# Optimization experiments

Hardware: AMD Instinct MI355X
Metric: run time of the kernel (lower is better)

The kernel has to match this reference:

```python
import jax, jax.numpy as jnp
import numpy as np

N = 100000
E = 1600000
H = 128
C = 40
BN_EPS = 1e-5


def setup_inputs() -> dict:
    key = jax.random.key(0)
    ks = jax.random.split(key, 8)
    x = jax.random.normal(ks[0], (N, H), dtype=jnp.float32)
    edge_index = jax.random.randint(ks[1], (2, E), 0, N, dtype=jnp.int64)
    # 3 GCN blocks (input + 2 hidden), all [H -> H] since in_channels == hidden_channels
    bn_gamma = jnp.ones((3, H), dtype=jnp.float32)
    bn_beta = jnp.zeros((3, H), dtype=jnp.float32)
    W = jax.random.normal(ks[2], (3, H, H), dtype=jnp.float32) / np.sqrt(H)
    b = jnp.zeros((3, H), dtype=jnp.float32)
    Wo = jax.random.normal(ks[3], (H, C), dtype=jnp.float32) / np.sqrt(H)
    bo = jnp.zeros((C,), dtype=jnp.float32)
    return {"x": x, "edge_index": edge_index, "bn_gamma": bn_gamma,
            "bn_beta": bn_beta, "W": W, "b": b, "Wo": Wo, "bo": bo}


def _gcn_norm(edge_index):
    # add self-loops, compute symmetric normalization deg^-1/2 * deg^-1/2
    loop = jnp.arange(N, dtype=edge_index.dtype)
    src = jnp.concatenate([edge_index[0], loop])  # [E+N]
    dst = jnp.concatenate([edge_index[1], loop])
    deg = jax.ops.segment_sum(jnp.ones_like(dst, dtype=jnp.float32), dst, num_segments=N)
    dinv = jnp.where(deg > 0, jax.lax.rsqrt(deg), 0.0)
    norm = dinv[src] * dinv[dst]  # [E+N]
    return src, dst, norm


def _block(x, src, dst, norm, gamma, beta, Wl, bl):
    # Dropout(p=0.6) in eval mode -> identity
    # BatchNorm (batch statistics, biased var, eps=1e-5)
    mean = jnp.mean(x, axis=0)
    var = jnp.mean(jnp.square(x - mean), axis=0)
    x = gamma * (x - mean) * jax.lax.rsqrt(var + BN_EPS) + beta
    # GCNConv: linear transform then normalized scatter-add aggregation
    h = x @ Wl  # [N, H]
    msg = h[src] * norm[:, None]  # [E+N, H] gather + scale
    out = jax.ops.segment_sum(msg, dst, num_segments=N) + bl
    return jax.nn.relu(out)


def reference(x, edge_index, bn_gamma, bn_beta, W, b, Wo, bo):
    src, dst, norm = _gcn_norm(edge_index)
    for i in range(3):
        x = _block(x, src, dst, norm, bn_gamma[i], bn_beta[i], W[i], b[i])
    logits = x @ Wo + bo  # [N, C]
    return jnp.squeeze(logits)
```

## Files before the change

kernel.cpp:

```cpp
#include <hip/hip_runtime.h>
#include <hip/hip_bf16.h>
#include <hip/hip_fp16.h>
#include <cstdint>

#define HDIM 128
#define BN_EPS 1e-5f
#define SCAN_CHUNK 1024

typedef _Float16 hf2 __attribute__((ext_vector_type(2)));
typedef _Float16 hf8 __attribute__((ext_vector_type(8)));
typedef float f32x4 __attribute__((ext_vector_type(4)));

static inline size_t align256(size_t x) { return (x + 255) & ~size_t(255); }

__global__ void detect_kernel(const int* __restrict__ ebuf, int* __restrict__ flag) {
    __shared__ int r[256];
    int tid = threadIdx.x;
    int o = 0;
    for (int i = tid; i < 4096; i += 256) o |= ebuf[2 * i + 1];
    r[tid] = o;
    __syncthreads();
    for (int s = 128; s > 0; s >>= 1) {
        if (tid < s) r[tid] |= r[tid + s];
        __syncthreads();
    }
    if (tid == 0) *flag = (r[0] == 0) ? 1 : 0;
}

__device__ __forceinline__ void bn_finalize_body(int blk, int t,
                                                 const float* __restrict__ part, int rows,
                                                 const float* __restrict__ gamma,
                                                 const float* __restrict__ beta,
                                                 const float* __restrict__ W,
                                                 _Float16* __restrict__ Wf,
                                                 float* __restrict__ hbp, int n) {
    int c = t & 127, h = t >> 7;
    float s = 0.f, s2 = 0.f;
    for (int b = h; b < rows; b += 2) {
        float2 v = ((const float2*)part)[(size_t)b * 128 + c];
        s += v.x; s2 += v.y;
    }
    __shared__ float rS[2][HDIM], rQ[2][HDIM];
    __shared__ float scs[HDIM], shs[HDIM];
    rS[h][c] = s; rQ[h][c] = s2;
    __syncthreads();
    if (h == 0) {
        s += rS[1][c]; s2 += rQ[1][c];
        float mean = s / n;
        float var = s2 / n - mean * mean;
        float sc = gamma[c] * rsqrtf(var + BN_EPS);
        scs[c] = sc;
        shs[c] = beta[c] - mean * sc;
    }
    __syncthreads();
    float acc = 0.f;
    int tbase = (c >> 4) * 4;
    int nlane = c & 15;
    int k0 = blk * 16 + h * 8;
#pragma unroll
    for (int kk = 0; kk < 8; ++kk) {
        int k = k0 + kk;
        float w = W[k * HDIM + c];
        int idx = (((tbase + (k >> 5)) * 64) + (((k >> 3) & 3) * 16 + nlane)) * 8 + (k & 7);
        Wf[idx] = (_Float16)(scs[k] * w);
        acc += shs[k] * w;
    }
    hbp[(blk * 2 + h) * HDIM + c] = acc;
}

__global__ __launch_bounds__(256) void front_kernel(const int* __restrict__ ebuf,
                                                    const int* __restrict__ flag,
                                                    int* __restrict__ deg,
                                                    int* __restrict__ rank,
                                                    const float4* __restrict__ x4,
                                                    float* __restrict__ part,
                                                    int E, int n, int ge, int nbn) {
    int t = threadIdx.x;
    if ((int)blockIdx.x < ge) {
        int e = blockIdx.x * 256 + t;
        if (e >= E) return;
        int d = (*flag) ? ebuf[2 * (E + e)] : ebuf[E + e];
        rank[e] = atomicAdd(&deg[d], 1);
        return;
    }
    int b = blockIdx.x - ge;
    int c4 = t & 31;
    int rsub = t >> 5;
    int rowsPer = (n + nbn - 1) / nbn;
    int r0 = b * rowsPer, r1 = min(r0 + rowsPer, n);
    float s[4] = {0.f, 0.f, 0.f, 0.f}, q[4] = {0.f, 0.f, 0.f, 0.f};
    for (int r = r0 + rsub; r < r1; r += 8) {
        float4 v = x4[(size_t)r * 32 + c4];
        s[0] += v.x; q[0] += v.x * v.x;
        s[1] += v.y; q[1] += v.y * v.y;
        s[2] += v.z; q[2] += v.z * v.z;
        s[3] += v.w; q[3] += v.w * v.w;
    }
    __shared__ float sS[8][HDIM], sQ[8][HDIM];
#pragma unroll
    for (int j = 0; j < 4; ++j) { sS[rsub][c4 * 4 + j] = s[j]; sQ[rsub][c4 * 4 + j] = q[j]; }
    __syncthreads();
    if (t < HDIM) {
        float ss = 0.f, qq = 0.f;
#pragma unroll
        for (int k = 0; k < 8; ++k) { ss += sS[k][t]; qq += sQ[k][t]; }
        ((float2*)part)[(size_t)b * 128 + t] = make_float2(ss, qq);
    }
}

__global__ __launch_bounds__(256) void bn_reduce1(const float* __restrict__ part,
                                                  float* __restrict__ part2, int rows) {
    int t = threadIdx.x;
    int per = (rows + gridDim.x - 1) / gridDim.x;
    int b0 = blockIdx.x * per, b1 = min(b0 + per, rows);
    float acc = 0.f;
    for (int r = b0; r < b1; ++r) acc += part[(size_t)r * 256 + t];
    part2[(size_t)blockIdx.x * 256 + t] = acc;
}

__global__ __launch_bounds__(256) void scanp_fin(const int* __restrict__ deg,
                                                 int* __restrict__ bsum,
                                                 const float* __restrict__ part2, int rows,
                                                 const float* __restrict__ gamma,
                                                 const float* __restrict__ beta,
                                                 const float* __restrict__ W,
                                                 _Float16* __restrict__ Wf,
                                                 float* __restrict__ hbp,
                                                 int n, int nscan) {
    int t = threadIdx.x;
    if ((int)blockIdx.x < nscan) {
        int base = blockIdx.x * SCAN_CHUNK;
        int lane = t & 63, w = t >> 6;
        int s = 0;
#pragma unroll
        for (int i = 0; i < 4; ++i) {
            int idx = base + t + 256 * i;
            if (idx < n) s += deg[idx];
        }
#pragma unroll
        for (int off = 32; off > 0; off >>= 1) s += __shfl_down(s, off);
        __shared__ int wred[4];
        if (lane == 0) wred[w] = s;
        __syncthreads();
        if (t == 0) bsum[blockIdx.x] = wred[0] + wred[1] + wred[2] + wred[3];
        return;
    }
    bn_finalize_body(blockIdx.x - nscan, t, part2, rows, gamma, beta, W, Wf, hbp, n);
}

__global__ __launch_bounds__(256) void bn_finalize_k(const float* __restrict__ part, int rows,
                                                     const float* __restrict__ gamma,
                                                     const float* __restrict__ beta,
                                                     const float* __restrict__ W,
                                                     _Float16* __restrict__ Wf,
                                                     float* __restrict__ hbp, int n) {
    bn_finalize_body(blockIdx.x, threadIdx.x, part, rows, gamma, beta, W, Wf, hbp, n);
}

__global__ __launch_bounds__(128) void scan_offsets(const int* __restrict__ bsum,
                                                    int* __restrict__ bofs, int nb) {
    int t = threadIdx.x;
    int v = (t < nb) ? bsum[t] : 0;
    int x = v;
#pragma unroll
    for (int off = 1; off < 64; off <<= 1) {
        int y = __shfl_up(x, off);
        if ((t & 63) >= off) x += y;
    }
    __shared__ int w0tot;
    if (t == 63) w0tot = x;
    __syncthreads();
    int incl = x + ((t >= 64) ? w0tot : 0);
    if (t < nb) bofs[t] = incl - v;
}

__global__ __launch_bounds__(256) void scan_final(const int* __restrict__ deg,
                                                  const int* __restrict__ bofs,
                                                  int* __restrict__ row_ptr,
                                                  float* __restrict__ dinv, int n, int E) {
    int base = blockIdx.x * SCAN_CHUNK;
    int t = threadIdx.x, lane = t & 63, w = t >> 6;
    int d0[4]; int s = 0;
#pragma unroll
    for (int i = 0; i < 4; ++i) {
        int idx = base + t * 4 + i;
        d0[i] = (idx < n) ? deg[idx] : 0;
        s += d0[i];
    }
    int x = s;
#pragma unroll
    for (int off = 1; off < 64; off <<= 1) {
        int y = __shfl_up(x, off);
        if (lane >= off) x += y;
    }
    __shared__ int wsum[4];
    if (lane == 63) wsum[w] = x;
    __syncthreads();
    int woff = 0;
#pragma unroll
    for (int k = 0; k < 4; ++k) if (k < w) woff += wsum[k];
    int ex = x - s + woff + bofs[blockIdx.x];
#pragma unroll
    for (int i = 0; i < 4; ++i) {
        int idx = base + t * 4 + i;
        if (idx < n) {
            row_ptr[idx] = ex;
            dinv[idx] = rsqrtf((float)(d0[i] + 1));
            ex += d0[i];
        }
    }
    if (blockIdx.x == 0 && t == 0) row_ptr[n] = E;
}

__global__ void fill_csr(const int* __restrict__ ebuf, const int* __restrict__ flag,
                         const int* __restrict__ row_ptr, const int* __restrict__ rank,
                         int* __restrict__ csr_src, int E) {
    int base = blockIdx.x * 512 + threadIdx.x;
    bool f = (*flag != 0);
#pragma unroll
    for (int i = 0; i < 2; ++i) {
        int e = base + i * 256;
        if (e < E) {
            int s = f ? ebuf[2 * e] : ebuf[e];
            int d = f ? ebuf[2 * (E + e)] : ebuf[E + e];
            csr_src[row_ptr[d] + rank[e]] = s;
        }
    }
}

template<bool F16SRC>
__global__ __launch_bounds__(256) void gemm_mfma(const void* __restrict__ xsrc,
                                                 const _Float16* __restrict__ Wf,
                                                 const float* __restrict__ hbp,
                                                 const float* __restrict__ dinv,
                                                 __half* __restrict__ Q, int n) {
    constexpr int XS = 136;
    __shared__ _Float16 xs[128 * XS];
    __shared__ float dvs[128];
    __shared__ float hbs[128];
    int t = threadIdx.x;
    int rowBase = blockIdx.x * 128;
    if (t < 128) {
        int gr = rowBase + t;
        dvs[t] = (gr < n) ? dinv[gr] : 0.f;
        float hsum = 0.f;
#pragma unroll
        for (int b = 0; b < 16; ++b) hsum += hbp[b * HDIM + t];
        hbs[t] = hsum;
    }
    int wid = t >> 6, l = t & 63;
    int wm = wid >> 1, wn = wid & 1;
    const hf8* wf8 = (const hf8*)Wf;
    hf8 bf[4][4];
#pragma unroll
    for (int i = 0; i < 4; ++i)
#pragma unroll
        for (int kk = 0; kk < 4; ++kk)
            bf[i][kk] = wf8[((4 * wn + i) * 4 + kk) * 64 + l];
    if (F16SRC) {
        const uint4* xg = (const uint4*)xsrc;
#pragma unroll
        for (int i = 0; i < 8; ++i) {
            int idx = t + 256 * i;
            int row = idx >> 4, o4 = idx & 15;
            int gr = rowBase + row;
            uint4 v = make_uint4(0, 0, 0, 0);
            if (gr < n) v = xg[(size_t)gr * 16 + o4];
            *(uint4*)&xs[row * XS + o4 * 8] = v;
        }
    } else {
        const float4* xg = (const float4*)xsrc;
#pragma unroll
        for (int i = 0; i < 16; ++i) {
            int idx = t + 256 * i;
            int row = idx >> 5, o = idx & 31;
            int gr = rowBase + row;
            float4 v = make_float4(0.f, 0.f, 0.f, 0.f);
            if (gr < n) v = xg[(size_t)gr * 32 + o];
            hf2 a; a.x = (_Float16)v.x; a.y = (_Float16)v.y;
            hf2 b; b.x = (_Float16)v.z; b.y = (_Float16)v.w;
            *(hf2*)&xs[row * XS + o * 4]     = a;
            *(hf2*)&xs[row * XS + o * 4 + 2] = b;
        }
    }
    __syncthreads();
    f32x4 acc[4][4] = {};
    int mlane = l & 15, agrp = l >> 4;
#pragma unroll
    for (int kk = 0; kk < 4; ++kk) {
        hf8 af[4];
#pragma unroll
        for (int mt = 0; mt < 4; ++mt)
            af[mt] = *(const hf8*)&xs[(64 * wm + 16 * mt + mlane) * XS + 32 * kk + 8 * agrp];
#pragma unroll
        for (int mt = 0; mt < 4; ++mt)
#pragma unroll
            for (int i = 0; i < 4; ++i)
                acc[mt][i] = __builtin_amdgcn_mfma_f32_16x16x32_f16(af[mt], bf[i][kk],
                                                                    acc[mt][i], 0, 0, 0);
    }
#pragma unroll
    for (int mt = 0; mt < 4; ++mt) {
        int r0 = 64 * wm + 16 * mt + agrp * 4;
#pragma unroll
        for (int j = 0; j < 4; ++j) {
            int r = r0 + j;
            int grow = rowBase + r;
            if (grow < n) {
                float dv = dvs[r];
#pragma unroll
                for (int i = 0; i < 4; ++i) {
                    int c = 16 * (4 * wn + i) + mlane;
                    Q[(size_t)grow * 128 + c] = __float2half(dv * (acc[mt][i][j] + hbs[c]));
                }
            }
        }
    }
}

__device__ __forceinline__ void add8(float acc[8], uint4 v) {
    const __half2* p = (const __half2*)&v;
#pragma unroll
    for (int j = 0; j < 4; ++j) {
        float2 f = __half22float2(p[j]);
        acc[2 * j]     += f.x;
        acc[2 * j + 1] += f.y;
    }
}

__global__ __launch_bounds__(256) void agg_kernel(const __half* __restrict__ h,
                                                  const int* __restrict__ row_ptr,
                                                  const int* __restrict__ csr_src,
                                                  const float* __restrict__ dinv,
                                                  const float* __restrict__ bias,
                                                  __half* __restrict__ xn,
                                                  float* __restrict__ part, int n) {
    int t = threadIdx.x;
    int lane16 = t & 15;
    int g = t >> 4;
    int d = blockIdx.x * 16 + g;
    bool active = (d < n);
    const uint4* h4 = (const uint4*)h;
    float v[8];
#pragma unroll
    for (int j = 0; j < 8; ++j) v[j] = 0.f;
    if (active) {
        float acc[8];
        {
            uint4 hv = h4[(size_t)d * 16 + lane16];
            const __half2* p = (const __half2*)&hv;
#pragma unroll
            for (int j = 0; j < 4; ++j) {
                float2 f = __half22float2(p[j]);
                acc[2 * j]     = f.x;
                acc[2 * j + 1] = f.y;
            }
        }
        int e0 = row_ptr[d], e1 = row_ptr[d + 1];
        int e = e0;
        for (; e + 16 <= e1; e += 16) {
            int idx[16];
#pragma unroll
            for (int i = 0; i < 16; ++i) idx[i] = csr_src[e + i];
            uint4 vv[16];
#pragma unroll
            for (int i = 0; i < 16; ++i) vv[i] = h4[(size_t)idx[i] * 16 + lane16];
#pragma unroll
            for (int i = 0; i < 16; ++i) add8(acc, vv[i]);
        }
        int rem = e1 - e;
        if (rem > 0) {
            int idx[16];
#pragma unroll
            for (int i = 0; i < 16; ++i)
                if (i < rem) idx[i] = csr_src[e + i];
            uint4 vv[16];
#pragma unroll
            for (int i = 0; i < 16; ++i)
                if (i < rem) vv[i] = h4[(size_t)idx[i] * 16 + lane16];
#pragma unroll
            for (int i = 0; i < 16; ++i)
                if (i < rem) add8(acc, vv[i]);
        }
        float dv = dinv[d];
        const float4* bb = (const float4*)(bias + lane16 * 8);
        float4 b0 = bb[0], b1 = bb[1];
        v[0] = fmaxf(fmaf(dv, acc[0], b0.x), 0.f);
        v[1] = fmaxf(fmaf(dv, acc[1], b0.y), 0.f);
        v[2] = fmaxf(fmaf(dv, acc[2], b0.z), 0.f);
        v[3] = fmaxf(fmaf(dv, acc[3], b0.w), 0.f);
        v[4] = fmaxf(fmaf(dv, acc[4], b1.x), 0.f);
        v[5] = fmaxf(fmaf(dv, acc[5], b1.y), 0.f);
        v[6] = fmaxf(fmaf(dv, acc[6], b1.z), 0.f);
        v[7] = fmaxf(fmaf(dv, acc[7], b1.w), 0.f);
        union { uint4 u; __half2 h2[4]; } o;
        o.h2[0] = __floats2half2_rn(v[0], v[1]);
        o.h2[1] = __floats2half2_rn(v[2], v[3]);
        o.h2[2] = __floats2half2_rn(v[4], v[5]);
        o.h2[3] = __floats2half2_rn(v[6], v[7]);
        ((uint4*)xn)[(size_t)d * 16 + lane16] = o.u;
    }
    if (part) {
        __shared__ float redS[16][HDIM];
        __shared__ float redQ[16][HDIM];
#pragma unroll
        for (int j = 0; j < 8; ++j) {
            redS[g][lane16 * 8 + j] = v[j];
            redQ[g][lane16 * 8 + j] = v[j] * v[j];
        }
        __syncthreads();
        if (t < HDIM) {
            float s = 0.f, q = 0.f;
#pragma unroll
            for (int k = 0; k < 16; ++k) { s += redS[k][t]; q += redQ[k][t]; }
            ((float2*)part)[(size_t)blockIdx.x * 128 + t] = make_float2(s, q);
        }
    }
}

__global__ __launch_bounds__(320) void gemm_out(const __half* __restrict__ x,
                                                const float* __restrict__ Wo,
                                                const float* __restrict__ bo,
                                                float* __restrict__ out, int n, int C) {
    __shared__ __align__(16) float wls[HDIM * 40];
    __shared__ __align__(16) float xs[32 * HDIM];
    __shared__ float bos[40];
    int t = threadIdx.x;
    for (int i = t; i < HDIM * 40; i += 320) wls[i] = Wo[i];
    if (t < 40) bos[t] = bo[t];
    int c = t % 40, lr = t / 40;
    int rowBase = blockIdx.x * 32;
    const uint4* xg = (const uint4*)x;
    for (int i = t; i < 512; i += 320) {
        int row = i >> 4, o4 = i & 15;
        int gr = rowBase + row;
        uint4 v = make_uint4(0, 0, 0, 0);
        if (gr < n) v = xg[(size_t)gr * 16 + o4];
        union { uint4 u; __half2 h2[4]; } cv; cv.u = v;
        float2 f0 = __half22float2(cv.h2[0]);
        float2 f1 = __half22float2(cv.h2[1]);
        float2 f2 = __half22float2(cv.h2[2]);
        float2 f3 = __half22float2(cv.h2[3]);
        ((float4*)xs)[i * 2]     = make_float4(f0.x, f0.y, f1.x, f1.y);
        ((float4*)xs)[i * 2 + 1] = make_float4(f2.x, f2.y, f3.x, f3.y);
    }
    __syncthreads();
    const float4* xsr0 = (const float4*)(xs + (lr + 0) * HDIM);
    const float4* xsr1 = (const float4*)(xs + (lr + 8) * HDIM);
    const float4* xsr2 = (const float4*)(xs + (lr + 16) * HDIM);
    const float4* xsr3 = (const float4*)(xs + (lr + 24) * HDIM);
    float acc0 = 0.f, acc1 = 0.f, acc2 = 0.f, acc3 = 0.f;
#pragma unroll 4
    for (int k4 = 0; k4 < 32; ++k4) {
        float4 xv0 = xsr0[k4], xv1 = xsr1[k4], xv2 = xsr2[k4], xv3 = xsr3[k4];
#define OSTEP(kk, e0, e1, e2, e3)                          \
        {                                                   \
            float wv = wls[(k4 * 4 + kk) * 40 + c];         \
            acc0 = fmaf(e0, wv, acc0);                      \
            acc1 = fmaf(e1, wv, acc1);                      \
            acc2 = fmaf(e2, wv, acc2);                      \
            acc3 = fmaf(e3, wv, acc3);                      \
        }
        OSTEP(0, xv0.x, xv1.x, xv2.x, xv3.x)
        OSTEP(1, xv0.y, xv1.y, xv2.y, xv3.y)
        OSTEP(2, xv0.z, xv1.z, xv2.z, xv3.z)
        OSTEP(3, xv0.w, xv1.w, xv2.w, xv3.w)
#undef OSTEP
    }
    float bb = bos[c];
    int g0 = rowBase + lr;
    if (g0 < n)      out[(size_t)g0 * 40 + c]        = acc0 + bb;
    if (g0 + 8 < n)  out[(size_t)(g0 + 8) * 40 + c]  = acc1 + bb;
    if (g0 + 16 < n) out[(size_t)(g0 + 16) * 40 + c] = acc2 + bb;
    if (g0 + 24 < n) out[(size_t)(g0 + 24) * 40 + c] = acc3 + bb;
}

extern "C" void kernel_launch(void* const* d_in, const int* in_sizes, int n_in,
                              void* d_out, int out_size, void* d_ws, size_t ws_size,
                              hipStream_t stream) {
    const float* x_in  = (const float*)d_in[0];
    const int*   ebuf  = (const int*)d_in[1];
    const float* gamma = (const float*)d_in[2];
    const float* beta  = (const float*)d_in[3];
    const float* Wall  = (const float*)d_in[4];
    const float* ball  = (const float*)d_in[5];
    const float* Wo    = (const float*)d_in[6];
    const float* bo    = (const float*)d_in[7];
    float* out = (float*)d_out;
    const int N = in_sizes[0] / HDIM;
    const int E = in_sizes[1] / 2;
    const int C = 40;

    char* base = (char*)d_ws;
    size_t off = 0;
    auto alloc = [&](size_t bytes) -> void* {
        void* p = base + off;
        off = align256(off + bytes);
        return p;
    };
    const int g_agg = (N + 15) / 16;
    const int g_bn0 = 1024;
    int part_rows = (g_agg > g_bn0) ? g_agg : g_bn0;
    __half*   Xh0     = (__half*)alloc((size_t)N * HDIM * 2);
    __half*   Xh1     = (__half*)alloc((size_t)N * HDIM * 2);
    __half*   Q       = (__half*)alloc((size_t)N * HDIM * 2);
    int*      csr_src = (int*)alloc((size_t)E * 4);
    int*      rank    = (int*)alloc((size_t)E * 4);
    int*      deg     = (int*)alloc((size_t)N * 4);
    float*    dinv    = (float*)alloc((size_t)N * 4);
    int*      row_ptr = (int*)alloc((size_t)(N + 1) * 4);
    float*    part    = (float*)alloc((size_t)part_rows * 256 * 4);
    float*    part2   = (float*)alloc((size_t)64 * 256 * 4);
    _Float16* Wf      = (_Float16*)alloc((size_t)HDIM * HDIM * 2);
    float*    hbp     = (float*)alloc((size_t)16 * HDIM * 4);
    int*      bsum    = (int*)alloc((size_t)256 * 4);
    int*      bofs    = (int*)alloc((size_t)256 * 4);
    int*      flag    = (int*)alloc(4);

    hipMemsetAsync(deg, 0, (size_t)N * 4, stream);
    detect_kernel<<<1, 256, 0, stream>>>(ebuf, flag);
    int ge = (E + 255) / 256;
    int nscan = (N + SCAN_CHUNK - 1) / SCAN_CHUNK;

    front_kernel<<<ge + g_bn0, 256, 0, stream>>>(ebuf, flag, deg, rank,
                                                 (const float4*)x_in, part, E, N, ge, g_bn0);
    bn_reduce1<<<64, 256, 0, stream>>>(part, part2, g_bn0);
    scanp_fin<<<nscan + 8, 256, 0, stream>>>(deg, bsum, part2, 64,
                                             gamma, beta, Wall, Wf, hbp, N, nscan);
    scan_offsets<<<1, 128, 0, stream>>>(bsum, bofs, nscan);
    scan_final<<<nscan, 256, 0, stream>>>(deg, bofs, row_ptr, dinv, N, E);
    fill_csr<<<(E + 511) / 512, 256, 0, stream>>>(ebuf, flag, row_ptr, rank, csr_src, E);

    int gg = (N + 127) / 128;
    for (int l = 0; l < 3; ++l) {
        const void* xc = (l == 0) ? (const void*)x_in
                                  : (l == 1) ? (const void*)Xh0 : (const void*)Xh1;
        __half* xn = (l == 0) ? Xh0 : (l == 1) ? Xh1 : Xh0;
        if (l > 0) {
            bn_reduce1<<<64, 256, 0, stream>>>(part, part2, g_agg);
            bn_finalize_k<<<8, 256, 0, stream>>>(part2, 64, gamma + l * HDIM, beta + l * HDIM,
                                                 Wall + (size_t)l * HDIM * HDIM, Wf, hbp, N);
        }
        if (l == 0) gemm_mfma<false><<<gg, 256, 0, stream>>>(xc, Wf, hbp, dinv, Q, N);
        else        gemm_mfma<true ><<<gg, 256, 0, stream>>>(xc, Wf, hbp, dinv, Q, N);
        float* statp = (l < 2) ? part : nullptr;
        agg_kernel<<<g_agg, 256, 0, stream>>>(Q, row_ptr, csr_src, dinv,
                                              ball + l * HDIM, xn, statp, N);
    }
    gemm_out<<<(N + 31) / 32, 320, 0, stream>>>(Xh0, Wo, bo, out, N, C);
}
```

Measured before the change: 474.3 us.

## Merge preprocessing launches: fuse memset with detect, scan offsets, fill with first GEMM

```diff
diff --git a/kernel.cpp b/kernel.cpp
--- a/kernel.cpp
+++ b/kernel.cpp
@@ -13,7 +13,13 @@
 
 static inline size_t align256(size_t x) { return (x + 255) & ~size_t(255); }
 
-__global__ void detect_kernel(const int* __restrict__ ebuf, int* __restrict__ flag) {
+__global__ void detect_zero(const int* __restrict__ ebuf, int* __restrict__ flag,
+                            int* __restrict__ deg, int n) {
+    if (blockIdx.x > 0) {
+        int i = (blockIdx.x - 1) * 256 + threadIdx.x;
+        if (i < n) deg[i] = 0;
+        return;
+    }
     __shared__ int r[256];
     int tid = threadIdx.x;
     int o = 0;
@@ -157,29 +163,21 @@
     bn_finalize_body(blockIdx.x, threadIdx.x, part, rows, gamma, beta, W, Wf, hbp, n);
 }
 
-__global__ __launch_bounds__(128) void scan_offsets(const int* __restrict__ bsum,
-                                                    int* __restrict__ bofs, int nb) {
-    int t = threadIdx.x;
-    int v = (t < nb) ? bsum[t] : 0;
-    int x = v;
-#pragma unroll
-    for (int off = 1; off < 64; off <<= 1) {
-        int y = __shfl_up(x, off);
-        if ((t & 63) >= off) x += y;
-    }
-    __shared__ int w0tot;
-    if (t == 63) w0tot = x;
-    __syncthreads();
-    int incl = x + ((t >= 64) ? w0tot : 0);
-    if (t < nb) bofs[t] = incl - v;
-}
-
-__global__ __launch_bounds__(256) void scan_final(const int* __restrict__ deg,
-                                                  const int* __restrict__ bofs,
-                                                  int* __restrict__ row_ptr,
-                                                  float* __restrict__ dinv, int n, int E) {
+__global__ __launch_bounds__(256) void scan_final2(const int* __restrict__ deg,
+                                                   const int* __restrict__ bsum,
+                                                   int* __restrict__ row_ptr,
+                                                   float* __restrict__ dinv,
+                                                   int n, int E) {
+    int t = threadIdx.x, lane = t & 63, w = t >> 6;
+    __shared__ int ored[4];
+    int v = (t < (int)blockIdx.x) ? bsum[t] : 0;
+#pragma unroll
+    for (int off = 32; off > 0; off >>= 1) v += __shfl_down(v, off);
+    if (lane == 0) ored[w] = v;
+    __syncthreads();
+    int bofs = ored[0] + ored[1] + ored[2] + ored[3];
+
     int base = blockIdx.x * SCAN_CHUNK;
-    int t = threadIdx.x, lane = t & 63, w = t >> 6;
     int d0[4]; int s = 0;
 #pragma unroll
     for (int i = 0; i < 4; ++i) {
@@ -199,7 +197,7 @@
     int woff = 0;
 #pragma unroll
     for (int k = 0; k < 4; ++k) if (k < w) woff += wsum[k];
-    int ex = x - s + woff + bofs[blockIdx.x];
+    int ex = x - s + woff + bofs;
 #pragma unroll
     for (int i = 0; i < 4; ++i) {
         int idx = base + t * 4 + i;
@@ -212,34 +210,18 @@
     if (blockIdx.x == 0 && t == 0) row_ptr[n] = E;
 }
 
-__global__ void fill_csr(const int* __restrict__ ebuf, const int* __restrict__ flag,
-                         const int* __restrict__ row_ptr, const int* __restrict__ rank,
-                         int* __restrict__ csr_src, int E) {
-    int base = blockIdx.x * 512 + threadIdx.x;
-    bool f = (*flag != 0);
-#pragma unroll
-    for (int i = 0; i < 2; ++i) {
-        int e = base + i * 256;
-        if (e < E) {
-            int s = f ? ebuf[2 * e] : ebuf[e];
-            int d = f ? ebuf[2 * (E + e)] : ebuf[E + e];
-            csr_src[row_ptr[d] + rank[e]] = s;
-        }
-    }
-}
-
 template<bool F16SRC>
-__global__ __launch_bounds__(256) void gemm_mfma(const void* __restrict__ xsrc,
-                                                 const _Float16* __restrict__ Wf,
-                                                 const float* __restrict__ hbp,
-                                                 const float* __restrict__ dinv,
-                                                 __half* __restrict__ Q, int n) {
+__device__ __forceinline__ void gemm_body(int bid, int t,
+                                          const void* __restrict__ xsrc,
+                                          const _Float16* __restrict__ Wf,
+                                          const float* __restrict__ hbp,
+                                          const float* __restrict__ dinv,
+                                          __half* __restrict__ Q, int n) {
     constexpr int XS = 136;
     __shared__ _Float16 xs[128 * XS];
     __shared__ float dvs[128];
     __shared__ float hbs[128];
-    int t = threadIdx.x;
-    int rowBase = blockIdx.x * 128;
+    int rowBase = bid * 128;
     if (t < 128) {
         int gr = rowBase + t;
         dvs[t] = (gr < n) ? dinv[gr] : 0.f;
@@ -316,6 +298,44 @@
             }
         }
     }
+}
+
+template<bool F16SRC>
+__global__ __launch_bounds__(256) void gemm_mfma(const void* __restrict__ xsrc,
+                                                 const _Float16* __restrict__ Wf,
+                                                 const float* __restrict__ hbp,
+                                                 const float* __restrict__ dinv,
+                                                 __half* __restrict__ Q, int n) {
+    gemm_body<F16SRC>(blockIdx.x, threadIdx.x, xsrc, Wf, hbp, dinv, Q, n);
+}
+
+__global__ __launch_bounds__(256) void fill_gemm0(const int* __restrict__ ebuf,
+                                                  const int* __restrict__ flag,
+                                                  const int* __restrict__ row_ptr,
+                                                  const int* __restrict__ rank,
+                                                  int* __restrict__ csr_src, int E,
+                                                  const void* __restrict__ xsrc,
+                                                  const _Float16* __restrict__ Wf,
+                                                  const float* __restrict__ hbp,
+                                                  const float* __restrict__ dinv,
+                                                  __half* __restrict__ Q, int n,
+                                                  int gfill) {
+    int t = threadIdx.x;
+    if ((int)blockIdx.x < gfill) {
+        int base = blockIdx.x * 512 + t;
+        bool f = (*flag != 0);
+#pragma unroll
+        for (int i = 0; i < 2; ++i) {
+            int e = base + i * 256;
+            if (e < E) {
+                int s = f ? ebuf[2 * e] : ebuf[e];
+                int d = f ? ebuf[2 * (E + e)] : ebuf[E + e];
+                csr_src[row_ptr[d] + rank[e]] = s;
+            }
+        }
+        return;
+    }
+    gemm_body<false>(blockIdx.x - gfill, t, xsrc, Wf, hbp, dinv, Q, n);
 }
 
 __device__ __forceinline__ void add8(float acc[8], uint4 v) {
@@ -514,35 +534,32 @@
     _Float16* Wf      = (_Float16*)alloc((size_t)HDIM * HDIM * 2);
     float*    hbp     = (float*)alloc((size_t)16 * HDIM * 4);
     int*      bsum    = (int*)alloc((size_t)256 * 4);
-    int*      bofs    = (int*)alloc((size_t)256 * 4);
     int*      flag    = (int*)alloc(4);
 
-    hipMemsetAsync(deg, 0, (size_t)N * 4, stream);
-    detect_kernel<<<1, 256, 0, stream>>>(ebuf, flag);
     int ge = (E + 255) / 256;
     int nscan = (N + SCAN_CHUNK - 1) / SCAN_CHUNK;
 
+    detect_zero<<<1 + (N + 255) / 256, 256, 0, stream>>>(ebuf, flag, deg, N);
     front_kernel<<<ge + g_bn0, 256, 0, stream>>>(ebuf, flag, deg, rank,
                                                  (const float4*)x_in, part, E, N, ge, g_bn0);
     bn_reduce1<<<64, 256, 0, stream>>>(part, part2, g_bn0);
     scanp_fin<<<nscan + 8, 256, 0, stream>>>(deg, bsum, part2, 64,
                                              gamma, beta, Wall, Wf, hbp, N, nscan);
-    scan_offsets<<<1, 128, 0, stream>>>(bsum, bofs, nscan);
-    scan_final<<<nscan, 256, 0, stream>>>(deg, bofs, row_ptr, dinv, N, E);
-    fill_csr<<<(E + 511) / 512, 256, 0, stream>>>(ebuf, flag, row_ptr, rank, csr_src, E);
-
+    scan_final2<<<nscan, 256, 0, stream>>>(deg, bsum, row_ptr, dinv, N, E);
+    int gfill = (E + 511) / 512;
     int gg = (N + 127) / 128;
+    fill_gemm0<<<gfill + gg, 256, 0, stream>>>(ebuf, flag, row_ptr, rank, csr_src, E,
+                                               x_in, Wf, hbp, dinv, Q, N, gfill);
+
     for (int l = 0; l < 3; ++l) {
-        const void* xc = (l == 0) ? (const void*)x_in
-                                  : (l == 1) ? (const void*)Xh0 : (const void*)Xh1;
         __half* xn = (l == 0) ? Xh0 : (l == 1) ? Xh1 : Xh0;
         if (l > 0) {
+            const void* xc = (l == 1) ? (const void*)Xh0 : (const void*)Xh1;
             bn_reduce1<<<64, 256, 0, stream>>>(part, part2, g_agg);
             bn_finalize_k<<<8, 256, 0, stream>>>(part2, 64, gamma + l * HDIM, beta + l * HDIM,
                                                  Wall + (size_t)l * HDIM * HDIM, Wf, hbp, N);
-        }
-        if (l == 0) gemm_mfma<false><<<gg, 256, 0, stream>>>(xc, Wf, hbp, dinv, Q, N);
-        else        gemm_mfma<true ><<<gg, 256, 0, stream>>>(xc, Wf, hbp, dinv, Q, N);
+            gemm_mfma<true><<<gg, 256, 0, stream>>>(xc, Wf, hbp, dinv, Q, N);
+        }
         float* statp = (l < 2) ? part : nullptr;
         agg_kernel<<<g_agg, 256, 0, stream>>>(Q, row_ptr, csr_src, dinv,
                                               ball + l * HDIM, xn, statp, N);
```

After: 463.9 us. -2.2%, faster.
